# Optimization experiments

Measured on AMD Instinct MI355X. Metric: run time of the kernel, lower is better.

The kernel has to match this reference:

```python
import jax, jax.numpy as jnp
import numpy as np

B, S, D = 1, 2048, 2048
N_HEAD, N_KV = 32, 8
HD = D // N_HEAD  # 64


def make_freqs_cis(seq_len, head_dim, base=10000.0):
    inv = 1.0 / (base ** (np.arange(0, head_dim, 2, dtype=np.float32) / head_dim))
    t = np.arange(seq_len, dtype=np.float32)
    f = np.outer(t, inv)  # [S, HD/2]
    return jnp.asarray(np.stack([np.cos(f), np.sin(f)], axis=-1))  # [S, HD/2, 2]


def setup_inputs() -> dict:
    key = jax.random.key(0)
    k1, k2, k3 = jax.random.split(key, 3)
    scale = 1.0 / np.sqrt(D)
    return {
        "hidden_states": jax.random.normal(k1, (B, S, D), jnp.float32),
        "freqs_cis": make_freqs_cis(S, HD),
        "wqkv": jax.random.normal(k2, ((N_HEAD + 2 * N_KV) * HD, D), jnp.float32) * scale,
        "wo": jax.random.normal(k3, (D, D), jnp.float32) * scale,
    }


def apply_rotary(x, freqs_cis):
    # x: [B, S, H, HD]; freqs_cis: [S, HD/2, 2]
    xs = x.reshape(*x.shape[:-1], HD // 2, 2)
    cos = freqs_cis[None, :, None, :, 0]
    sin = freqs_cis[None, :, None, :, 1]
    x0, x1 = xs[..., 0], xs[..., 1]
    out = jnp.stack([x0 * cos - x1 * sin, x1 * cos + x0 * sin], axis=-1)
    return out.reshape(x.shape)


def reference(hidden_states, freqs_cis, wqkv, wo):
    bsz, seq_len, _ = hidden_states.shape
    kv_size = N_KV * HD
    qkv = hidden_states @ wqkv.T  # [B, S, 3072]
    q, k, v = jnp.split(qkv, [D, D + kv_size], axis=-1)
    q = q.reshape(bsz, seq_len, N_HEAD, HD)
    k = k.reshape(bsz, seq_len, N_KV, HD)
    v = v.reshape(bsz, seq_len, N_KV, HD)
    q = apply_rotary(q, freqs_cis)
    k = apply_rotary(k, freqs_cis)
    # [B, H, S, HD]
    q = q.transpose(0, 2, 1, 3)
    k = k.transpose(0, 2, 1, 3)
    v = v.transpose(0, 2, 1, 3)
    rep = N_HEAD // N_KV
    k = jnp.repeat(k, rep, axis=1)
    v = jnp.repeat(v, rep, axis=1)
    scores = jnp.einsum("bhqd,bhkd->bhqk", q, k) / jnp.sqrt(jnp.float32(HD))
    causal = jnp.tril(jnp.ones((seq_len, seq_len), bool))
    scores = jnp.where(causal[None, None], scores, jnp.finfo(scores.dtype).min)
    attn = jax.nn.softmax(scores, axis=-1)
    out = jnp.einsum("bhqk,bhkd->bhqd", attn, v)
    out = out.transpose(0, 2, 1, 3).reshape(bsz, seq_len, D)
    return out @ wo.T
```

## Files before the change

### kernel.cpp

```cpp
#include <hip/hip_runtime.h>

typedef unsigned short u16;
typedef __attribute__((ext_vector_type(8))) short bf16x8;
typedef __attribute__((ext_vector_type(4))) float f32x4;

#define MFMA16(a, b, c) __builtin_amdgcn_mfma_f32_16x16x32_bf16((a), (b), (c), 0, 0, 0)
#define EXP2(x) __builtin_amdgcn_exp2f(x)

#define S 2048
#define D 2048
#define NH 32
#define NKV 8
#define HD 64
#define QKV_N 3072

__device__ __forceinline__ u16 f2bf(float f) {
  unsigned int u = __float_as_uint(f);
  u += 0x7fffu + ((u >> 16) & 1u);
  return (u16)(u >> 16);
}

__device__ __forceinline__ void glds16(const void* g, void* l) {
  __builtin_amdgcn_global_load_lds((const __attribute__((address_space(1))) unsigned int*)g,
                                   (__attribute__((address_space(3))) unsigned int*)l,
                                   16, 0, 0);
}

#define N1 (S * D / 4)
#define N2 (QKV_N * D / 4)
#define N3 (D * D / 4)
__global__ void cast_all(const float* __restrict__ hs, const float* __restrict__ wqkv,
                         const float* __restrict__ wo, u16* __restrict__ o1,
                         u16* __restrict__ o2, u16* __restrict__ o3) {
  int i = blockIdx.x * blockDim.x + threadIdx.x;
  const float* src;
  u16* dst;
  int idx;
  if (i < N1) { src = hs; dst = o1; idx = i; }
  else if (i < N1 + N2) { src = wqkv; dst = o2; idx = i - N1; }
  else if (i < N1 + N2 + N3) { src = wo; dst = o3; idx = i - N1 - N2; }
  else return;
  float4 v = ((const float4*)src)[idx];
  ushort4 o;
  o.x = f2bf(v.x); o.y = f2bf(v.y); o.z = f2bf(v.z); o.w = f2bf(v.w);
  ((ushort4*)dst)[idx] = o;
}

#define GEMM_MAINLOOP(A_, B_, K_, bm_, bn_)                                            \
  const int srowS = lane >> 3, scolS = ((lane & 7) ^ srowS) * 8;                       \
  const int aBase = wave * 32, bBase = wave * 16;                                      \
  const int qq = lane >> 4, sw = lr & 7;                                               \
  _Pragma("unroll") for (int c2 = 0; c2 < 4; ++c2)                                     \
      glds16(A_ + (size_t)(bm_ + aBase + c2 * 8 + srowS) * K_ + scolS,                 \
             &sA[0][aBase + c2 * 8][0]);                                               \
  _Pragma("unroll") for (int c2 = 0; c2 < 2; ++c2)                                     \
      glds16(B_ + (size_t)(bn_ + bBase + c2 * 8 + srowS) * K_ + scolS,                 \
             &sB[0][bBase + c2 * 8][0]);                                               \
  const int nk = K_ >> 6;                                                              \
  for (int it = 0; it < nk; ++it) {                                                    \
    const int buf = it & 1;                                                            \
    __syncthreads();                                                                   \
    if (it + 1 < nk) {                                                                 \
      const int k1 = (it + 1) << 6;                                                    \
      _Pragma("unroll") for (int c2 = 0; c2 < 4; ++c2)                                 \
          glds16(A_ + (size_t)(bm_ + aBase + c2 * 8 + srowS) * K_ + k1 + scolS,        \
                 &sA[buf ^ 1][aBase + c2 * 8][0]);                                     \
      _Pragma("unroll") for (int c2 = 0; c2 < 2; ++c2)                                 \
          glds16(B_ + (size_t)(bn_ + bBase + c2 * 8 + srowS) * K_ + k1 + scolS,        \
                 &sB[buf ^ 1][bBase + c2 * 8][0]);                                     \
    }                                                                                  \
    bf16x8 af[2][2], bfr[2][4];                                                        \
    _Pragma("unroll") for (int c = 0; c < 2; ++c) {                                    \
      const int pc = (((c << 2) | qq) ^ sw) * 8;     \
      _Pragma("unroll") for (int i = 0; i < 2; ++i)                                    \
          af[c][i] = *(const bf16x8*)(&sA[buf][wr + i * 16 + lr][pc]);                 \
      _Pragma("unroll") for (int j = 0; j < 4; ++j)                                    \
          bfr[c][j] = *(const bf16x8*)(&sB[buf][j * 16 + lr][pc]);                     \
    }                                                                                  \
    _Pragma("unroll") for (int c = 0; c < 2; ++c)                                      \
        _Pragma("unroll") for (int i = 0; i < 2; ++i)                                  \
            _Pragma("unroll") for (int j = 0; j < 4; ++j)                              \
                acc[i][j] = MFMA16(af[c][i], bfr[c][j], acc[i][j]);                    \
  }

__global__ __launch_bounds__(256) void gemm_bt(const u16* __restrict__ A, const u16* __restrict__ B,
                                               float* __restrict__ C, int M, int N, int K) {
  __shared__ u16 sA[2][128][64];
  __shared__ u16 sB[2][64][64];
  const int tid = threadIdx.x;
  const int wave = tid >> 6, lane = tid & 63;
  const int bm = blockIdx.y * 128, bn = blockIdx.x * 64;
  const int lr = lane & 15, lk = (lane >> 4) * 8;
  const int wr = wave * 32;
  (void)lk;

  f32x4 acc[2][4] = {};
  GEMM_MAINLOOP(A, B, K, bm, bn)

  const int crb = (lane >> 4) * 4;
#pragma unroll
  for (int i = 0; i < 2; ++i)
#pragma unroll
    for (int j = 0; j < 4; ++j)
#pragma unroll
      for (int r = 0; r < 4; ++r) {
        int row = bm + wr + i * 16 + crb + r;
        int col = bn + j * 16 + lr;
        C[(size_t)row * N + col] = acc[i][j][r];
      }
}

#define QSCALE 0.18033688011112042f
__global__ __launch_bounds__(256) void gemm1_fused(const u16* __restrict__ A, const u16* __restrict__ B,
                                                   const float* __restrict__ fc,
                                                   u16* __restrict__ qo, u16* __restrict__ ko,
                                                   u16* __restrict__ vt) {
  __shared__ u16 sA[2][128][64];
  __shared__ u16 sB[2][64][64];
  const int tid = threadIdx.x;
  const int wave = tid >> 6, lane = tid & 63;
  const int bm = blockIdx.y * 128, bn = blockIdx.x * 64;
  const int lr = lane & 15, lk = (lane >> 4) * 8;
  const int wr = wave * 32;
  (void)lk;

  f32x4 acc[2][4] = {};
  GEMM_MAINLOOP(A, B, D, bm, bn)

  const int crb = (lane >> 4) * 4;

  if (bn < 2560) {
    const bool isQ = (bn < 2048);
    u16* dst_base = isQ ? (qo + (size_t)(bn >> 6) * S * HD)
                        : (ko + (size_t)((bn - 2048) >> 6) * S * HD);
    const float scale = isQ ? QSCALE : 1.0f;
    const int odd = lr & 1;
#pragma unroll
    for (int i = 0; i < 2; ++i)
#pragma unroll
      for (int r = 0; r < 4; ++r) {
        const int srow = bm + wr + i * 16 + crb + r;
#pragma unroll
        for (int j = 0; j < 4; ++j) {
          const int d = j * 16 + lr;
          float x = acc[i][j][r];
          float xp = __shfl_xor(x, 1, 64);
          float2 cs = *(const float2*)(fc + (size_t)srow * 64 + (d >> 1) * 2);
          float y = odd ? (x * cs.x + xp * cs.y) : (x * cs.x - xp * cs.y);
          dst_base[(size_t)srow * HD + d] = f2bf(y * scale);
        }
      }
  } else {
    const int kvh = (bn - 2560) >> 6;
    __syncthreads();
    u16(*sT)[136] = (u16(*)[136]) & sA[0][0][0];
#pragma unroll
    for (int i = 0; i < 2; ++i)
#pragma unroll
      for (int j = 0; j < 4; ++j)
#pragma unroll
        for (int r = 0; r < 4; ++r)
          sT[j * 16 + lr][wr + i * 16 + crb + r] = f2bf(acc[i][j][r]);
    __syncthreads();
    const int d = tid >> 2, sc = (tid & 3) * 32;
    uint4* dst = (uint4*)(vt + (size_t)kvh * HD * S + (size_t)d * S + bm + sc);
    const uint4* src = (const uint4*)(&sT[d][sc]);
    dst[0] = src[0];
    dst[1] = src[1];
    dst[2] = src[2];
    dst[3] = src[3];
  }
}

__global__ __launch_bounds__(256) void attn_kernel(const u16* __restrict__ Q, const u16* __restrict__ Kc,
                                                   const u16* __restrict__ Vt, u16* __restrict__ Out) {
  __shared__ u16 sK[64][72];
  __shared__ u16 sV[64][72];
  __shared__ u16 sP[4][16][68];

  const int p = blockIdx.x;
  const int h = blockIdx.y;
  const int kvh = h >> 2;
  const int tid = threadIdx.x;
  const int wave = tid >> 6, lane = tid & 63;
  const int lr = lane & 15;
  const int lk = (lane >> 4) * 8;
  const int crb = (lane >> 4) * 4;
  const int t = 4 * p + wave;
  const int qbA = 16 * t;
  const int qbB = 16 * (127 - t);

  const u16* qpA = Q + ((size_t)h * S + qbA + lr) * HD;
  const u16* qpB = Q + ((size_t)h * S + qbB + lr) * HD;
  bf16x8 aA0 = *(const bf16x8*)(qpA + lk);
  bf16x8 aA1 = *(const bf16x8*)(qpA + 32 + lk);
  bf16x8 aB0 = *(const bf16x8*)(qpB + lk);
  bf16x8 aB1 = *(const bf16x8*)(qpB + 32 + lk);

  const u16* Kh = Kc + (size_t)kvh * S * HD;
  const u16* Vh = Vt + (size_t)kvh * HD * S;

  const int sr0 = tid >> 3, so0 = (tid & 7) * 8;
  const int sr1 = sr0 + 32;

  float lA[4] = {0.f, 0.f, 0.f, 0.f}, lB[4] = {0.f, 0.f, 0.f, 0.f};
  f32x4 oA[4] = {}, oB[4] = {};

  const int kend = (32 - p) * 64;

  uint4 pk0 = *(const uint4*)(Kh + (size_t)sr0 * HD + so0);
  uint4 pk1 = *(const uint4*)(Kh + (size_t)sr1 * HD + so0);
  uint4 pv0 = *(const uint4*)(Vh + (size_t)sr0 * S + so0);
  uint4 pv1 = *(const uint4*)(Vh + (size_t)sr1 * S + so0);

  for (int kb = 0; kb < kend; kb += 64) {
    *(uint4*)(&sK[sr0][so0]) = pk0;
    *(uint4*)(&sK[sr1][so0]) = pk1;
    *(uint4*)(&sV[sr0][so0]) = pv0;
    *(uint4*)(&sV[sr1][so0]) = pv1;
    __syncthreads();

    const int kn = kb + 64;
    if (kn < kend) {
      pk0 = *(const uint4*)(Kh + (size_t)(kn + sr0) * HD + so0);
      pk1 = *(const uint4*)(Kh + (size_t)(kn + sr1) * HD + so0);
      pv0 = *(const uint4*)(Vh + (size_t)sr0 * S + kn + so0);
      pv1 = *(const uint4*)(Vh + (size_t)sr1 * S + kn + so0);
    }

    const bool liveA = (kb <= qbA + 15);

    f32x4 cA[4], cB[4];
#pragma unroll
    for (int tt = 0; tt < 4; ++tt) {
      bf16x8 b0 = *(const bf16x8*)(&sK[tt * 16 + lr][lk]);
      bf16x8 b1 = *(const bf16x8*)(&sK[tt * 16 + lr][32 + lk]);
      f32x4 zB = {};
      zB = MFMA16(aB0, b0, zB);
      cB[tt] = MFMA16(aB1, b1, zB);
      if (liveA) {
        f32x4 zA = {};
        zA = MFMA16(aA0, b0, zA);
        cA[tt] = MFMA16(aA1, b1, zA);
      }
    }

    if (kb + 63 <= qbB) {
#pragma unroll
      for (int r = 0; r < 4; ++r)
#pragma unroll
        for (int tt = 0; tt < 4; ++tt) {
          float pp = EXP2(cB[tt][r] - 8.0f);
          lB[r] += pp;
          sP[wave][crb + r][tt * 16 + lr] = f2bf(pp);
        }
    } else {
#pragma unroll
      for (int r = 0; r < 4; ++r) {
        const int qr = qbB + crb + r;
#pragma unroll
        for (int tt = 0; tt < 4; ++tt) {
          float pp = (kb + tt * 16 + lr <= qr) ? EXP2(cB[tt][r] - 8.0f) : 0.0f;
          lB[r] += pp;
          sP[wave][crb + r][tt * 16 + lr] = f2bf(pp);
        }
      }
    }
    {
      bf16x8 pb0 = *(const bf16x8*)(&sP[wave][lr][lk]);
      bf16x8 pb1 = *(const bf16x8*)(&sP[wave][lr][32 + lk]);
#pragma unroll
      for (int tt = 0; tt < 4; ++tt) {
        bf16x8 v0 = *(const bf16x8*)(&sV[tt * 16 + lr][lk]);
        bf16x8 v1 = *(const bf16x8*)(&sV[tt * 16 + lr][32 + lk]);
        oB[tt] = MFMA16(pb0, v0, oB[tt]);
        oB[tt] = MFMA16(pb1, v1, oB[tt]);
      }
    }

    if (liveA) {
      if (kb + 63 <= qbA) {
#pragma unroll
        for (int r = 0; r < 4; ++r)
#pragma unroll
          for (int tt = 0; tt < 4; ++tt) {
            float pp = EXP2(cA[tt][r] - 8.0f);
            lA[r] += pp;
            sP[wave][crb + r][tt * 16 + lr] = f2bf(pp);
          }
      } else {
#pragma unroll
        for (int r = 0; r < 4; ++r) {
          const int qr = qbA + crb + r;
#pragma unroll
          for (int tt = 0; tt < 4; ++tt) {
            float pp = (kb + tt * 16 + lr <= qr) ? EXP2(cA[tt][r] - 8.0f) : 0.0f;
            lA[r] += pp;
            sP[wave][crb + r][tt * 16 + lr] = f2bf(pp);
          }
        }
      }
      bf16x8 pa0 = *(const bf16x8*)(&sP[wave][lr][lk]);
      bf16x8 pa1 = *(const bf16x8*)(&sP[wave][lr][32 + lk]);
#pragma unroll
      for (int tt = 0; tt < 4; ++tt) {
        bf16x8 v0 = *(const bf16x8*)(&sV[tt * 16 + lr][lk]);
        bf16x8 v1 = *(const bf16x8*)(&sV[tt * 16 + lr][32 + lk]);
        oA[tt] = MFMA16(pa0, v0, oA[tt]);
        oA[tt] = MFMA16(pa1, v1, oA[tt]);
      }
    }
    __syncthreads();
  }

#pragma unroll
  for (int r = 0; r < 4; ++r) {
#pragma unroll
    for (int off = 1; off < 16; off <<= 1) {
      lA[r] += __shfl_xor(lA[r], off, 64);
      lB[r] += __shfl_xor(lB[r], off, 64);
    }
    lA[r] = 1.0f / lA[r];
    lB[r] = 1.0f / lB[r];
  }
#pragma unroll
  for (int tt = 0; tt < 4; ++tt)
#pragma unroll
    for (int r = 0; r < 4; ++r) {
      const int d = tt * 16 + lr;
      Out[(size_t)(qbA + crb + r) * D + h * HD + d] = f2bf(oA[tt][r] * lA[r]);
      Out[(size_t)(qbB + crb + r) * D + h * HD + d] = f2bf(oB[tt][r] * lB[r]);
    }
}

extern "C" void kernel_launch(void* const* d_in, const int* in_sizes, int n_in,
                              void* d_out, int out_size, void* d_ws, size_t ws_size,
                              hipStream_t stream) {
  const float* hs = (const float*)d_in[0];
  const float* fc = (const float*)d_in[1];
  const float* wqkv = (const float*)d_in[2];
  const float* wo = (const float*)d_in[3];
  float* out = (float*)d_out;
  char* ws = (char*)d_ws;

  u16* hs_bf   = (u16*)(ws);
  u16* wqkv_bf = (u16*)(ws + ((size_t)8 << 20));
  u16* wo_bf   = (u16*)(ws + ((size_t)20 << 20));
  u16* q_bf    = (u16*)(ws + ((size_t)28 << 20));
  u16* k_bf    = (u16*)(ws + ((size_t)36 << 20));
  u16* vt_bf   = (u16*)(ws + ((size_t)38 << 20));
  u16* attn_bf = (u16*)(ws + ((size_t)40 << 20));

  cast_all<<<(N1 + N2 + N3 + 255) / 256, 256, 0, stream>>>(hs, wqkv, wo, hs_bf, wqkv_bf, wo_bf);

  gemm1_fused<<<dim3(QKV_N / 64, S / 128), 256, 0, stream>>>(hs_bf, wqkv_bf, fc, q_bf, k_bf, vt_bf);

  attn_kernel<<<dim3(16, NH), 256, 0, stream>>>(q_bf, k_bf, vt_bf, attn_bf);

  gemm_bt<<<dim3(D / 64, S / 128), 256, 0, stream>>>(attn_bf, wo_bf, out, S, D, D);
}
```

Baseline: 211.0 us.

## Software-pipeline PV matmul by one iteration with register-held P and V fragments

```diff
diff --git a/kernel.cpp b/kernel.cpp
--- a/kernel.cpp
+++ b/kernel.cpp
@@ -172,11 +172,11 @@
   }
 }
 
-__global__ __launch_bounds__(256) void attn_kernel(const u16* __restrict__ Q, const u16* __restrict__ Kc,
-                                                   const u16* __restrict__ Vt, u16* __restrict__ Out) {
+__global__ __launch_bounds__(256, 2) void attn_kernel(const u16* __restrict__ Q, const u16* __restrict__ Kc,
+                                                      const u16* __restrict__ Vt, u16* __restrict__ Out) {
   __shared__ u16 sK[64][72];
   __shared__ u16 sV[64][72];
-  __shared__ u16 sP[4][16][68];
+  __shared__ u16 sP[4][2][16][72];
 
   const int p = blockIdx.x;
   const int h = blockIdx.y;
@@ -213,7 +213,26 @@
   uint4 pv0 = *(const uint4*)(Vh + (size_t)sr0 * S + so0);
   uint4 pv1 = *(const uint4*)(Vh + (size_t)sr1 * S + so0);
 
+  bf16x8 vf[4][2];
+  bf16x8 pfB[2], pfA[2];
+  bool prevA = false;
+
   for (int kb = 0; kb < kend; kb += 64) {
+    if (kb > 0) {
+#pragma unroll
+      for (int tt = 0; tt < 4; ++tt) {
+        oB[tt] = MFMA16(pfB[0], vf[tt][0], oB[tt]);
+        oB[tt] = MFMA16(pfB[1], vf[tt][1], oB[tt]);
+      }
+      if (prevA) {
+#pragma unroll
+        for (int tt = 0; tt < 4; ++tt) {
+          oA[tt] = MFMA16(pfA[0], vf[tt][0], oA[tt]);
+          oA[tt] = MFMA16(pfA[1], vf[tt][1], oA[tt]);
+        }
+      }
+    }
+
     *(uint4*)(&sK[sr0][so0]) = pk0;
     *(uint4*)(&sK[sr1][so0]) = pk1;
     *(uint4*)(&sV[sr0][so0]) = pv0;
@@ -252,7 +271,7 @@
         for (int tt = 0; tt < 4; ++tt) {
           float pp = EXP2(cB[tt][r] - 8.0f);
           lB[r] += pp;
-          sP[wave][crb + r][tt * 16 + lr] = f2bf(pp);
+          sP[wave][0][crb + r][tt * 16 + lr] = f2bf(pp);
         }
     } else {
 #pragma unroll
@@ -262,19 +281,8 @@
         for (int tt = 0; tt < 4; ++tt) {
           float pp = (kb + tt * 16 + lr <= qr) ? EXP2(cB[tt][r] - 8.0f) : 0.0f;
           lB[r] += pp;
-          sP[wave][crb + r][tt * 16 + lr] = f2bf(pp);
-        }
-      }
-    }
-    {
-      bf16x8 pb0 = *(const bf16x8*)(&sP[wave][lr][lk]);
-      bf16x8 pb1 = *(const bf16x8*)(&sP[wave][lr][32 + lk]);
-#pragma unroll
-      for (int tt = 0; tt < 4; ++tt) {
-        bf16x8 v0 = *(const bf16x8*)(&sV[tt * 16 + lr][lk]);
-        bf16x8 v1 = *(const bf16x8*)(&sV[tt * 16 + lr][32 + lk]);
-        oB[tt] = MFMA16(pb0, v0, oB[tt]);
-        oB[tt] = MFMA16(pb1, v1, oB[tt]);
+          sP[wave][0][crb + r][tt * 16 + lr] = f2bf(pp);
+        }
       }
     }
 
@@ -286,7 +294,7 @@
           for (int tt = 0; tt < 4; ++tt) {
             float pp = EXP2(cA[tt][r] - 8.0f);
             lA[r] += pp;
-            sP[wave][crb + r][tt * 16 + lr] = f2bf(pp);
+            sP[wave][1][crb + r][tt * 16 + lr] = f2bf(pp);
           }
       } else {
 #pragma unroll
@@ -296,21 +304,38 @@
           for (int tt = 0; tt < 4; ++tt) {
             float pp = (kb + tt * 16 + lr <= qr) ? EXP2(cA[tt][r] - 8.0f) : 0.0f;
             lA[r] += pp;
-            sP[wave][crb + r][tt * 16 + lr] = f2bf(pp);
+            sP[wave][1][crb + r][tt * 16 + lr] = f2bf(pp);
           }
         }
       }
-      bf16x8 pa0 = *(const bf16x8*)(&sP[wave][lr][lk]);
-      bf16x8 pa1 = *(const bf16x8*)(&sP[wave][lr][32 + lk]);
-#pragma unroll
-      for (int tt = 0; tt < 4; ++tt) {
-        bf16x8 v0 = *(const bf16x8*)(&sV[tt * 16 + lr][lk]);
-        bf16x8 v1 = *(const bf16x8*)(&sV[tt * 16 + lr][32 + lk]);
-        oA[tt] = MFMA16(pa0, v0, oA[tt]);
-        oA[tt] = MFMA16(pa1, v1, oA[tt]);
-      }
-    }
+    }
+
+    pfB[0] = *(const bf16x8*)(&sP[wave][0][lr][lk]);
+    pfB[1] = *(const bf16x8*)(&sP[wave][0][lr][32 + lk]);
+    if (liveA) {
+      pfA[0] = *(const bf16x8*)(&sP[wave][1][lr][lk]);
+      pfA[1] = *(const bf16x8*)(&sP[wave][1][lr][32 + lk]);
+    }
+#pragma unroll
+    for (int tt = 0; tt < 4; ++tt) {
+      vf[tt][0] = *(const bf16x8*)(&sV[tt * 16 + lr][lk]);
+      vf[tt][1] = *(const bf16x8*)(&sV[tt * 16 + lr][32 + lk]);
+    }
+    prevA = liveA;
     __syncthreads();
+  }
+
+#pragma unroll
+  for (int tt = 0; tt < 4; ++tt) {
+    oB[tt] = MFMA16(pfB[0], vf[tt][0], oB[tt]);
+    oB[tt] = MFMA16(pfB[1], vf[tt][1], oB[tt]);
+  }
+  if (prevA) {
+#pragma unroll
+    for (int tt = 0; tt < 4; ++tt) {
+      oA[tt] = MFMA16(pfA[0], vf[tt][0], oA[tt]);
+      oA[tt] = MFMA16(pfA[1], vf[tt][1], oA[tt]);
+    }
   }
 
 #pragma unroll
```

Result: faster. 204.6 us (-3.0%).
